# Kernel tuning notes

Measured on AMD Instinct MI355X. Metric: run time of the kernel, lower is better.

## Reference

```python
import jax, jax.numpy as jnp
import numpy as np

NEG_SLOPE = 0.2
NUM_GRAPHS = 64


def _gatv2_layer(x, src, dst, Wl, bl, Wr, br, att, bias, n_nodes, heads, ch):
    # lin_l (source) and lin_r (target) transforms -> [N, H, C]
    xs = (x @ Wl + bl).reshape(n_nodes, heads, ch)
    xd = (x @ Wr + br).reshape(n_nodes, heads, ch)
    s = xs[src]                                   # [E, H, C] gathered source feats
    e = jax.nn.leaky_relu(s + xd[dst], NEG_SLOPE)  # GATv2: leaky_relu BEFORE att dot
    score = jnp.einsum('ehc,hc->eh', e, att)       # [E, H]
    # segment softmax over edges sharing the same target node
    smax = jax.ops.segment_max(score, dst, num_segments=n_nodes)
    ex = jnp.exp(score - smax[dst])
    denom = jax.ops.segment_sum(ex, dst, num_segments=n_nodes)
    alpha = ex / denom[dst]                        # [E, H]
    out = jax.ops.segment_sum(alpha[:, :, None] * s, dst, num_segments=n_nodes)
    return out.reshape(n_nodes, heads * ch) + bias


def setup_inputs() -> dict:
    key = jax.random.key(0)
    ks = jax.random.split(key, 20)
    N, E, F = 50000, 800000, 128
    H, C = 4, 64
    G = NUM_GRAPHS
    sc = 0.05
    inp = {
        'x': jax.random.normal(ks[0], (N, F), jnp.float32),
        'edge_index': jax.random.randint(ks[1], (2, E), 0, N, jnp.int64 if jax.config.read('jax_enable_x64') else jnp.int32).astype(jnp.int32),
        'batch': jnp.sort(jax.random.randint(ks[2], (N,), 0, G)).astype(jnp.int32),
        'W_l1': jax.random.normal(ks[3], (F, H * C)) * sc,
        'b_l1': jax.random.normal(ks[4], (H * C,)) * sc,
        'W_r1': jax.random.normal(ks[5], (F, H * C)) * sc,
        'b_r1': jax.random.normal(ks[6], (H * C,)) * sc,
        'att1': jax.random.normal(ks[7], (H, C)) * sc,
        'bias1': jax.random.normal(ks[8], (H * C,)) * sc,
        'W_l2': jax.random.normal(ks[9], (H * C, C)) * sc,
        'b_l2': jax.random.normal(ks[10], (C,)) * sc,
        'W_r2': jax.random.normal(ks[11], (H * C, C)) * sc,
        'b_r2': jax.random.normal(ks[12], (C,)) * sc,
        'att2': jax.random.normal(ks[13], (1, C)) * sc,
        'bias2': jax.random.normal(ks[14], (C,)) * sc,
        'W_lin': jax.random.normal(ks[15], (C, 1)) * sc,
        'b_lin': jax.random.normal(ks[16], (1,)) * sc,
    }
    return inp


def reference(x, edge_index, batch, W_l1, b_l1, W_r1, b_r1, att1, bias1,
              W_l2, b_l2, W_r2, b_r2, att2, bias2, W_lin, b_lin):
    N = x.shape[0]
    # PyG GATv2Conv adds self-loops by default
    loops = jnp.arange(N, dtype=edge_index.dtype)
    src = jnp.concatenate([edge_index[0], loops])
    dst = jnp.concatenate([edge_index[1], loops])

    h = _gatv2_layer(x, src, dst, W_l1, b_l1, W_r1, b_r1, att1, bias1, N, 4, 64)
    h = jax.nn.relu(h)  # dropout=identity (eval), norm=Identity
    h = _gatv2_layer(h, src, dst, W_l2, b_l2, W_r2, b_r2, att2, bias2, N, 1, 64)

    # global mean pool over graphs
    sums = jax.ops.segment_sum(h, batch, num_segments=NUM_GRAPHS)
    counts = jax.ops.segment_sum(jnp.ones((N,), h.dtype), batch, num_segments=NUM_GRAPHS)
    pooled = sums / jnp.maximum(counts, 1.0)[:, None]  # [G, 64]
    return pooled @ W_lin + b_lin                      # [G, 1]
```

## Files before the change

kernel.cpp:

```cpp
#include <hip/hip_runtime.h>
#include <hip/hip_bf16.h>
#include <math.h>

typedef __attribute__((ext_vector_type(8))) short short8;
typedef __attribute__((ext_vector_type(4))) float floatx4;
typedef __attribute__((ext_vector_type(4))) int intx4;

#define ATT_SCALE 0.865617024533378f
#define C_ABS 0.6666666666667f
#define PCLAMP 86.5f

__device__ __forceinline__ float bf2f(unsigned short u) {
  union { unsigned int i; float f; } v; v.i = ((unsigned int)u) << 16; return v.f;
}
__device__ __forceinline__ unsigned short f2bf(float f) {
  union { float f; unsigned int u; } v; v.f = f;
  unsigned int r = (v.u + 0x7fffu + ((v.u >> 16) & 1u)) >> 16;
  return (unsigned short)r;
}
__device__ __forceinline__ int imin(int a, int b) { return a < b ? a : b; }
__device__ __forceinline__ int iclamp(int v, int lo, int hi) {
  return v < lo ? lo : (v > hi ? hi : v);
}
__device__ __forceinline__ float uasf(unsigned int u) {
  union { unsigned int i; float f; } v; v.i = u; return v.f;
}
__device__ __forceinline__ float exp2fast(float x) {
#if __has_builtin(__builtin_amdgcn_exp2f)
  return __builtin_amdgcn_exp2f(x);
#else
  return exp2f(x);
#endif
}
__device__ __forceinline__ float sum16(float x) {
  union { float f; int i; } a, t;
  a.f = x;
  t.i = __builtin_amdgcn_update_dpp(0, a.i, 0x121, 0xF, 0xF, true); a.f += t.f;
  t.i = __builtin_amdgcn_update_dpp(0, a.i, 0x122, 0xF, 0xF, true); a.f += t.f;
  t.i = __builtin_amdgcn_update_dpp(0, a.i, 0x124, 0xF, 0xF, true); a.f += t.f;
  t.i = __builtin_amdgcn_update_dpp(0, a.i, 0x128, 0xF, 0xF, true); a.f += t.f;
  return a.f;
}

__global__ void k_sentinel(float* out, float val) {
  if (threadIdx.x < 64) out[threadIdx.x] = val;
}

struct CvtSegs {
  const void* src[10];
  unsigned short* dst[10];
  int len[10];
};

__global__ void k_prep(const void* __restrict__ x, unsigned short* __restrict__ x_c,
                       int n8, CvtSegs segs,
                       const void* __restrict__ s0, const void* __restrict__ s1,
                       const void* __restrict__ s2, const void* __restrict__ s3,
                       unsigned short* __restrict__ d0, unsigned short* __restrict__ d1,
                       unsigned short* __restrict__ d2, unsigned short* __restrict__ d3,
                       const int* __restrict__ edst, int* deg, int E, int N,
                       int* dflag, float* __restrict__ att1s, float* __restrict__ att2s,
                       int nCvt8, int nTransB) {
  __shared__ int csh;
  if (threadIdx.x == 0) csh = 0;
  __syncthreads();
  {
    unsigned short u = ((const unsigned short*)x)[threadIdx.x];
    int e = (u >> 7) & 0xFF;
    atomicAdd(&csh, (u == 0) || (e >= 100 && e <= 145));
  }
  __syncthreads();
  int isf = (csh < 240);

  int b = blockIdx.x;
  if (b < nCvt8) {
    if (!isf) return;
    int i = b * 256 + threadIdx.x;
    if (i >= n8) return;
    const float* s = (const float*)x + (size_t)i * 8;
    ushort4 a, c;
    a.x = f2bf(s[0]); a.y = f2bf(s[1]); a.z = f2bf(s[2]); a.w = f2bf(s[3]);
    c.x = f2bf(s[4]); c.y = f2bf(s[5]); c.z = f2bf(s[6]); c.w = f2bf(s[7]);
    ((ushort4*)x_c)[i * 2] = a;
    ((ushort4*)x_c)[i * 2 + 1] = c;
    return;
  }
  b -= nCvt8;
  if (b < 10) {
    if (b == 0 && threadIdx.x == 0) dflag[0] = isf;
    int i = threadIdx.x;
    if (i < segs.len[b]) {
      float v = isf ? ((const float*)segs.src[b])[i]
                    : bf2f(((const unsigned short*)segs.src[b])[i]);
      segs.dst[b][i] = f2bf(v);
      if (b == 2) att1s[i] = v * ATT_SCALE;
      if (b == 6) att2s[i] = v * ATT_SCALE;
    }
    return;
  }
  b -= 10;
  if (b < nTransB) {
    int idx = b * 256 + threadIdx.x;
    const void* src; unsigned short* dst; int R, C, loc;
    if (idx < 32768)      { src = s0; dst = d0; R = 128; C = 256; loc = idx; }
    else if (idx < 65536) { src = s1; dst = d1; R = 128; C = 256; loc = idx - 32768; }
    else if (idx < 81920) { src = s2; dst = d2; R = 256; C = 64;  loc = idx - 65536; }
    else                  { src = s3; dst = d3; R = 256; C = 64;  loc = idx - 81920; }
    unsigned short u = isf ? f2bf(((const float*)src)[loc])
                           : ((const unsigned short*)src)[loc];
    int r = loc / C, cc = loc - r * C;
    dst[cc * R + r] = u;
    return;
  }
  b -= nTransB;
  int base = b * 1024 + threadIdx.x;
#pragma unroll
  for (int k = 0; k < 4; ++k) {
    int e = base + k * 256;
    if (e < E) atomicAdd(&deg[iclamp(edst[e], 0, N - 1)], 1);
  }
}

__global__ __launch_bounds__(1024) void k_scan1(const int* __restrict__ deg, int* bsum, int N) {
  __shared__ int sm[1024];
  int tid = threadIdx.x;
  int i = blockIdx.x * 1024 + tid;
  sm[tid] = (i < N) ? ((deg[i] + 4) & ~3) : 0;
  __syncthreads();
  for (int off = 512; off > 0; off >>= 1) {
    if (tid < off) sm[tid] += sm[tid + off];
    __syncthreads();
  }
  if (tid == 0) bsum[blockIdx.x] = sm[0];
}

__global__ __launch_bounds__(1024) void k_scan3(const int* __restrict__ deg,
                                                const int* __restrict__ bsum,
                                                int* rowptr, int* cursor, int N) {
  __shared__ int sm[1024];
  __shared__ int boff;
  int tid = threadIdx.x;
  if (tid == 0) {
    int r = 0;
    for (int b = 0; b < blockIdx.x; ++b) r += bsum[b];
    boff = r;
  }
  int i = blockIdx.x * 1024 + tid;
  int v = (i < N) ? ((deg[i] + 4) & ~3) : 0;
  sm[tid] = v;
  __syncthreads();
  for (int off = 1; off < 1024; off <<= 1) {
    int t = (tid >= off) ? sm[tid - off] : 0;
    __syncthreads();
    sm[tid] += t;
    __syncthreads();
  }
  if (i < N) {
    int ex = sm[tid] - v + boff;
    rowptr[i] = ex;
    cursor[i] = ex;
    if (i == N - 1) rowptr[N] = ex + v;
  }
}

template <int K, int CT, int RT>
__device__ __forceinline__ void gemm2r_body(
    int bx, int by, int tid,
    const unsigned short* __restrict__ A,
    const unsigned short* __restrict__ BTl, const unsigned short* __restrict__ BTr,
    const unsigned short* __restrict__ bl, const unsigned short* __restrict__ br,
    unsigned short* __restrict__ outl, unsigned short* __restrict__ outr,
    int Nrows, int M) {
  constexpr int KI = K / 32;
  int lane = tid & 63;
  int wave = tid >> 6;
  int r = lane & 15, q = lane >> 4;
  int col0 = by * (4 * CT * 16) + wave * (CT * 16);
  int row0 = bx * (16 * RT);
  short8 Bl[KI][CT], Br[KI][CT];
#pragma unroll
  for (int t = 0; t < CT; ++t) {
    const unsigned short* bpl = BTl + (size_t)(col0 + t * 16 + r) * K + q * 8;
    const unsigned short* bpr = BTr + (size_t)(col0 + t * 16 + r) * K + q * 8;
#pragma unroll
    for (int k = 0; k < KI; ++k) {
      Bl[k][t] = *reinterpret_cast<const short8*>(bpl + k * 32);
      Br[k][t] = *reinterpret_cast<const short8*>(bpr + k * 32);
    }
  }
  float bvl[CT], bvr[CT];
#pragma unroll
  for (int t = 0; t < CT; ++t) {
    bvl[t] = bf2f(bl[col0 + t * 16 + r]);
    bvr[t] = bf2f(br[col0 + t * 16 + r]);
  }
  short8 a[KI], an[KI];
  {
    int ar0 = imin(row0 + r, Nrows - 1);
    const unsigned short* Ap = A + (size_t)ar0 * K + q * 8;
#pragma unroll
    for (int k = 0; k < KI; ++k) a[k] = *reinterpret_cast<const short8*>(Ap + k * 32);
  }
  for (int rt = 0; rt < RT; ++rt) {
    if (rt + 1 < RT) {
      int arn = imin(row0 + (rt + 1) * 16 + r, Nrows - 1);
      const unsigned short* Apn = A + (size_t)arn * K + q * 8;
#pragma unroll
      for (int k = 0; k < KI; ++k) an[k] = *reinterpret_cast<const short8*>(Apn + k * 32);
    }
    floatx4 accl[CT], accr[CT];
#pragma unroll
    for (int t = 0; t < CT; ++t) {
      accl[t] = (floatx4){0.f, 0.f, 0.f, 0.f};
      accr[t] = (floatx4){0.f, 0.f, 0.f, 0.f};
    }
#pragma unroll
    for (int k = 0; k < KI; ++k) {
#pragma unroll
      for (int t = 0; t < CT; ++t) {
        accl[t] = __builtin_amdgcn_mfma_f32_16x16x32_bf16(a[k], Bl[k][t], accl[t], 0, 0, 0);
        accr[t] = __builtin_amdgcn_mfma_f32_16x16x32_bf16(a[k], Br[k][t], accr[t], 0, 0, 0);
      }
    }
#pragma unroll
    for (int t = 0; t < CT; ++t) {
      int col = col0 + t * 16 + r;
#pragma unroll
      for (int rr = 0; rr < 4; ++rr) {
        int row = row0 + rt * 16 + q * 4 + rr;
        if (row < Nrows) {
          outl[(size_t)row * M + col] = f2bf(accl[t][rr] + bvl[t]);
          outr[(size_t)row * M + col] = f2bf(accr[t][rr] + bvr[t]);
        }
      }
    }
#pragma unroll
    for (int k = 0; k < KI; ++k) a[k] = an[k];
  }
}

__global__ __launch_bounds__(256) void k_phase1(
    const unsigned short* __restrict__ A0, const unsigned short* __restrict__ A1,
    const int* __restrict__ dflag,
    const unsigned short* __restrict__ BTl, const unsigned short* __restrict__ BTr,
    const unsigned short* __restrict__ bl, const unsigned short* __restrict__ br,
    unsigned short* __restrict__ outl, unsigned short* __restrict__ outr,
    int Nrows, int M, int nG, int nS,
    const int* __restrict__ esrc, const int* __restrict__ edst,
    const int* __restrict__ rowptr, const int* __restrict__ deg,
    int* cursor, int* colx, int E, int N) {
  int b = blockIdx.x;
  int m2 = 2 * imin(nG, nS);
  bool isG;
  int idx;
  if (b < m2) { isG = (b & 1) == 0; idx = b >> 1; }
  else        { isG = nG > nS;      idx = imin(nG, nS) + (b - m2); }
  if (isG) {
    const unsigned short* A = dflag[0] ? A1 : A0;
    gemm2r_body<128, 2, 8>(idx >> 1, idx & 1, threadIdx.x, A, BTl, BTr, bl, br,
                           outl, outr, Nrows, M);
    return;
  }
  int ET = E + N;
  int ETcap = E + 4 * N;
  int base = idx * 1024 + threadIdx.x;
#pragma unroll
  for (int k = 0; k < 4; ++k) {
    int e = base + k * 256;
    if (e < ET) {
      if (e < E) {
        int s = iclamp(esrc[e], 0, N - 1), d = iclamp(edst[e], 0, N - 1);
        int pos = atomicAdd(&cursor[d], 1);
        colx[iclamp(pos, 0, ETcap - 1)] = s;
      } else {
        int i = e - E;
        int bg = rowptr[i];
        int en = bg + deg[i];
        colx[en] = i;
        int cap = rowptr[i + 1];
        for (int j = en + 1; j < cap; ++j) colx[j] = 0;
        if (i == N - 1) {
          for (int j = cap; j < cap + 16; ++j) colx[j] = 0;
        }
      }
    }
  }
}

__global__ __launch_bounds__(256) void k_gemm2r_l2(
    const unsigned short* __restrict__ A,
    const unsigned short* __restrict__ BTl, const unsigned short* __restrict__ BTr,
    const unsigned short* __restrict__ bl, const unsigned short* __restrict__ br,
    unsigned short* __restrict__ outl, unsigned short* __restrict__ outr,
    int Nrows, int M) {
  gemm2r_body<256, 1, 4>(blockIdx.x, 0, threadIdx.x, A, BTl, BTr, bl, br,
                         outl, outr, Nrows, M);
}

#define UNPACK2(u, v0, v1, v2, v3)          \
  v0 = uasf(u.x << 16); v1 = uasf(u.x & 0xffff0000u); \
  v2 = uasf(u.y << 16); v3 = uasf(u.y & 0xffff0000u);

#define AGG4(U0, U1, U2, U3, E0, F0)                                         \
  {                                                                          \
    float va0, va1, va2, va3, vb0, vb1, vb2, vb3;                            \
    float vc0, vc1, vc2, vc3, vd0, vd1, vd2, vd3;                            \
    UNPACK2(U0, va0, va1, va2, va3)                                          \
    UNPACK2(U1, vb0, vb1, vb2, vb3)                                          \
    UNPACK2(U2, vc0, vc1, vc2, vc3)                                          \
    UNPACK2(U3, vd0, vd1, vd2, vd3)                                          \
    float qa0 = fmaf(a0, va0, ad0), qa1 = fmaf(a1, va1, ad1);                \
    float qa2 = fmaf(a2, va2, ad2), qa3 = fmaf(a3, va3, ad3);                \
    float qb0 = fmaf(a0, vb0, ad0), qb1 = fmaf(a1, vb1, ad1);                \
    float qb2 = fmaf(a2, vb2, ad2), qb3 = fmaf(a3, vb3, ad3);                \
    float qc0 = fmaf(a0, vc0, ad0), qc1 = fmaf(a1, vc1, ad1);                \
    float qc2 = fmaf(a2, vc2, ad2), qc3 = fmaf(a3, vc3, ad3);                \
    float qd0 = fmaf(a0, vd0, ad0), qd1 = fmaf(a1, vd1, ad1);                \
    float qd2 = fmaf(a2, vd2, ad2), qd3 = fmaf(a3, vd3, ad3);                \
    float pa = (qa0 + qa1) + (qa2 + qa3);                                    \
    float pb = (qb0 + qb1) + (qb2 + qb3);                                    \
    float pc = (qc0 + qc1) + (qc2 + qc3);                                    \
    float pd = (qd0 + qd1) + (qd2 + qd3);                                    \
    pa = fmaf(c0, fabsf(qa0), pa); pa = fmaf(c1, fabsf(qa1), pa);            \
    pa = fmaf(c2, fabsf(qa2), pa); pa = fmaf(c3, fabsf(qa3), pa);            \
    pb = fmaf(c0, fabsf(qb0), pb); pb = fmaf(c1, fabsf(qb1), pb);            \
    pb = fmaf(c2, fabsf(qb2), pb); pb = fmaf(c3, fabsf(qb3), pb);            \
    pc = fmaf(c0, fabsf(qc0), pc); pc = fmaf(c1, fabsf(qc1), pc);            \
    pc = fmaf(c2, fabsf(qc2), pc); pc = fmaf(c3, fabsf(qc3), pc);            \
    pd = fmaf(c0, fabsf(qd0), pd); pd = fmaf(c1, fabsf(qd1), pd);            \
    pd = fmaf(c2, fabsf(qd2), pd); pd = fmaf(c3, fabsf(qd3), pd);            \
    pa = sum16(pa); pb = sum16(pb); pc = sum16(pc); pd = sum16(pd);          \
    float l0 = (F0) ? PCLAMP : (((E0) < end) ? PCLAMP : -INFINITY);          \
    float l1 = ((E0) + 1 < end) ? PCLAMP : -INFINITY;                        \
    float l2 = ((E0) + 2 < end) ? PCLAMP : -INFINITY;                        \
    float l3 = ((E0) + 3 < end) ? PCLAMP : -INFINITY;                        \
    pa = fminf(pa, l0); pb = fminf(pb, l1);                                  \
    pc = fminf(pc, l2); pd = fminf(pd, l3);                                  \
    float wa = exp2fast(pa), wb = exp2fast(pb);                              \
    float wc = exp2fast(pc), wd = exp2fast(pd);                              \
    l += (wa + wb) + (wc + wd);                                              \
    o0 = fmaf(wa, va0, o0); o0 = fmaf(wb, vb0, o0);                          \
    o0 = fmaf(wc, vc0, o0); o0 = fmaf(wd, vd0, o0);                          \
    o1 = fmaf(wa, va1, o1); o1 = fmaf(wb, vb1, o1);                          \
    o1 = fmaf(wc, vc1, o1); o1 = fmaf(wd, vd1, o1);                          \
    o2 = fmaf(wa, va2, o2); o2 = fmaf(wb, vb2, o2);                          \
    o2 = fmaf(wc, vc2, o2); o2 = fmaf(wd, vd2, o2);                          \
    o3 = fmaf(wa, va3, o3); o3 = fmaf(wb, vb3, o3);                          \
    o3 = fmaf(wc, vc3, o3); o3 = fmaf(wd, vd3, o3);                          \
  }

__global__ __launch_bounds__(256, 6) void k_agg_h4(
    const int* __restrict__ rowptr, const int* __restrict__ deg,
    const int* __restrict__ colx,
    const unsigned short* __restrict__ xs, const unsigned short* __restrict__ xd,
    const float* __restrict__ atts, const unsigned short* __restrict__ bias,
    unsigned short* __restrict__ hout, int N) {
  int lane = threadIdx.x & 63;
  int dst = (blockIdx.x * 256 + threadIdx.x) >> 6;
  if (dst >= N) return;
  int off = lane << 2;
  unsigned int off2 = (unsigned int)off * 2;
  const char* xsb = (const char*)xs;
  floatx4 av = *reinterpret_cast<const floatx4*>(atts + off);
  ushort4 du = *reinterpret_cast<const ushort4*>(xd + (size_t)dst * 256 + off);
  float a0 = av[0], a1 = av[1], a2 = av[2], a3 = av[3];
  float d0 = bf2f(du.x), d1 = bf2f(du.y), d2 = bf2f(du.z), d3 = bf2f(du.w);
  float ad0 = a0 * d0, ad1 = a1 * d1, ad2 = a2 * d2, ad3 = a3 * d3;
  float c0 = copysignf(C_ABS, a0), c1 = copysignf(C_ABS, a1);
  float c2 = copysignf(C_ABS, a2), c3 = copysignf(C_ABS, a3);
  float l = 0.f, o0 = 0.f, o1 = 0.f, o2 = 0.f, o3 = 0.f;
  int beg = __builtin_amdgcn_readfirstlane(rowptr[dst]);
  int cnt = __builtin_amdgcn_readfirstlane(deg[dst]) + 1;
  int end = beg + cnt;
#define GATH(p) (*(const uint2*)(xsb + (((unsigned)(p) << 9) + off2)))
  intx4 pA = *(const intx4*)(colx + beg);
  intx4 pB = *(const intx4*)(colx + beg + 4);
  uint2 ua = GATH(pA.x), ub = GATH(pA.y), uc = GATH(pA.z), ud = GATH(pA.w);
  uint2 ue = GATH(pB.x), uf = GATH(pB.y), ug = GATH(pB.z), uh = GATH(pB.w);
  for (int e = beg; e < end; e += 8) {
    intx4 pC = *(const intx4*)(colx + e + 8);
    intx4 pD = *(const intx4*)(colx + e + 12);
    AGG4(ua, ub, uc, ud, e, 1)
    ua = GATH(pC.x); ub = GATH(pC.y); uc = GATH(pC.z); ud = GATH(pC.w);
    AGG4(ue, uf, ug, uh, e + 4, 0)
    ue = GATH(pD.x); uf = GATH(pD.y); ug = GATH(pD.z); uh = GATH(pD.w);
  }
#undef GATH
  float rl = 1.0f / l;
  ushort4 bu = *reinterpret_cast<const ushort4*>(bias + off);
  ushort4 res;
  res.x = f2bf(fmaxf(fmaf(o0, rl, bf2f(bu.x)), 0.f));
  res.y = f2bf(fmaxf(fmaf(o1, rl, bf2f(bu.y)), 0.f));
  res.z = f2bf(fmaxf(fmaf(o2, rl, bf2f(bu.z)), 0.f));
  res.w = f2bf(fmaxf(fmaf(o3, rl, bf2f(bu.w)), 0.f));
  *reinterpret_cast<ushort4*>(hout + (size_t)dst * 256 + off) = res;
}

__global__ __launch_bounds__(256, 6) void k_agg_h1(
    const int* __restrict__ rowptr, const int* __restrict__ deg,
    const int* __restrict__ colx,
    const unsigned short* __restrict__ xs, const unsigned short* __restrict__ xd,
    const float* __restrict__ atts, const unsigned short* __restrict__ bias,
    float* __restrict__ hout, int N) {
  int lane = threadIdx.x & 63;
  int wid = (blockIdx.x * 256 + threadIdx.x) >> 6;
  int g = lane >> 4, sl = lane & 15;
  int dst = wid * 4 + g;
  bool valid = dst < N;
  int dsafe = valid ? dst : 0;
  int cb = sl << 2;
  unsigned int cb2 = (unsigned int)cb * 2;
  const char* xsb = (const char*)xs;
  floatx4 av = *reinterpret_cast<const floatx4*>(atts + cb);
  ushort4 du = *reinterpret_cast<const ushort4*>(xd + (size_t)dsafe * 64 + cb);
  float a0 = av[0], a1 = av[1], a2 = av[2], a3 = av[3];
  float d0 = bf2f(du.x), d1 = bf2f(du.y), d2 = bf2f(du.z), d3 = bf2f(du.w);
  float ad0 = a0 * d0, ad1 = a1 * d1, ad2 = a2 * d2, ad3 = a3 * d3;
  float c0 = copysignf(C_ABS, a0), c1 = copysignf(C_ABS, a1);
  float c2 = copysignf(C_ABS, a2), c3 = copysignf(C_ABS, a3);
  float l = 0.f, o0 = 0.f, o1 = 0.f, o2 = 0.f, o3 = 0.f;
  int beg = valid ? rowptr[dst] : 0;
  int end = beg + (valid ? deg[dst] + 1 : 0);
#define GATH(p) (*(const uint2*)(xsb + (((unsigned)(p) << 7) + cb2)))
  intx4 pA = *(const intx4*)(colx + beg);
  intx4 pB = *(const intx4*)(colx + beg + 4);
  uint2 ua = GATH(pA.x), ub = GATH(pA.y), uc = GATH(pA.z), ud = GATH(pA.w);
  uint2 ue = GATH(pB.x), uf = GATH(pB.y), ug = GATH(pB.z), uh = GATH(pB.w);
  for (int e = beg; e < end; e += 8) {
    intx4 pC = *(const intx4*)(colx + e + 8);
    intx4 pD = *(const intx4*)(colx + e + 12);
    AGG4(ua, ub, uc, ud, e, 1)
    ua = GATH(pC.x); ub = GATH(pC.y); uc = GATH(pC.z); ud = GATH(pC.w);
    AGG4(ue, uf, ug, uh, e + 4, 0)
    ue = GATH(pD.x); uf = GATH(pD.y); ug = GATH(pD.z); uh = GATH(pD.w);
  }
#undef GATH
  if (valid) {
    float rl = 1.0f / l;
    ushort4 bu = *reinterpret_cast<const ushort4*>(bias + cb);
    floatx4 res;
    res[0] = fmaf(o0, rl, bf2f(bu.x));
    res[1] = fmaf(o1, rl, bf2f(bu.y));
    res[2] = fmaf(o2, rl, bf2f(bu.z));
    res[3] = fmaf(o3, rl, bf2f(bu.w));
    *reinterpret_cast<floatx4*>(hout + (size_t)dst * 64 + cb) = res;
  }
}

__global__ __launch_bounds__(256) void k_pool(const float* __restrict__ h2,
                                              const int* __restrict__ batch,
                                              float* pool, int* cnt, int N) {
  int lane = threadIdx.x & 63;
  int wid = (blockIdx.x * 256 + threadIdx.x) >> 6;
  int n0 = wid * 32;
  if (n0 >= N) return;
  int nend = imin(n0 + 32, N);
  float acc = 0.f;
  int c = 0;
  int gcur = iclamp(batch[n0], 0, 63);
  for (int n = n0; n < nend; ++n) {
    int gg = iclamp(batch[n], 0, 63);
    if (gg != gcur) {
      atomicAdd(&pool[gcur * 64 + lane], acc);
      if (lane == 0) atomicAdd(&cnt[gcur], c);
      acc = 0.f; c = 0; gcur = gg;
    }
    acc += h2[(size_t)n * 64 + lane];
    c++;
  }
  atomicAdd(&pool[gcur * 64 + lane], acc);
  if (lane == 0) atomicAdd(&cnt[gcur], c);
}

__global__ void k_final(const float* __restrict__ pool, const int* __restrict__ cnt,
                        const unsigned short* __restrict__ Wlinc,
                        const unsigned short* __restrict__ blinc,
                        float* __restrict__ out) {
  int g = threadIdx.x;
  if (g >= 64) return;
  float inv = 1.f / fmaxf((float)cnt[g], 1.f);
  float s = 0.f;
  for (int c = 0; c < 64; ++c) s += pool[g * 64 + c] * bf2f(Wlinc[c]);
  out[g] = fmaf(s, inv, bf2f(blinc[0]));
}

extern "C" void kernel_launch(void* const* d_in, const int* in_sizes, int n_in,
                              void* d_out, int out_size, void* d_ws, size_t ws_size,
                              hipStream_t stream) {
  const void* x     = d_in[0];
  const int*  ei    = (const int*)d_in[1];
  const int*  batch = (const int*)d_in[2];
  const void* Wl1 = d_in[3];  const void* bl1 = d_in[4];
  const void* Wr1 = d_in[5];  const void* br1 = d_in[6];
  const void* att1 = d_in[7]; const void* bias1 = d_in[8];
  const void* Wl2 = d_in[9];  const void* bl2 = d_in[10];
  const void* Wr2 = d_in[11]; const void* br2 = d_in[12];
  const void* att2 = d_in[13]; const void* bias2 = d_in[14];
  const void* Wlin = d_in[15]; const void* blin = d_in[16];
  float* out = (float*)d_out;

  const int F = 128, HC = 256, C2 = 64;
  int N = in_sizes[0] / F;
  int E = in_sizes[1] / 2;
  int ET = E + N;
  const int* esrc = ei;
  const int* edst = ei + E;

  char* w = (char*)d_ws;
  auto alloc = [&](size_t bytes) {
    char* p = w;
    w += (bytes + 255) & ~(size_t)255;
    return p;
  };
  int* dflag  = (int*)alloc(4);
  int* rowptr = (int*)alloc((size_t)(N + 1) * 4);
  int* cursor = (int*)alloc((size_t)N * 4);
  int* bsum   = (int*)alloc(1024 * 4);
  int* colx   = (int*)alloc((size_t)(E + 4 * N + 16) * 4);
  unsigned short* smallc = (unsigned short*)alloc(4096);
  float* att1s = (float*)alloc(256 * 4);
  float* att2s = (float*)alloc(64 * 4);
  unsigned short* Wl1T = (unsigned short*)alloc((size_t)F * HC * 2);
  unsigned short* Wr1T = (unsigned short*)alloc((size_t)F * HC * 2);
  unsigned short* Wl2T = (unsigned short*)alloc((size_t)HC * C2 * 2);
  unsigned short* Wr2T = (unsigned short*)alloc((size_t)HC * C2 * 2);
  int* deg    = (int*)alloc((size_t)N * 4);
  float* pool = (float*)alloc(64 * 64 * 4);
  int* cnt    = (int*)alloc(64 * 4);
  unsigned short* xs1  = (unsigned short*)alloc((size_t)N * HC * 2);
  unsigned short* xd1  = (unsigned short*)alloc((size_t)N * HC * 2);
  unsigned short* h1   = (unsigned short*)alloc((size_t)N * HC * 2);
  size_t required = (size_t)(w - (char*)d_ws);
  size_t zlen = (size_t)((char*)cnt + 256 - (char*)deg);

  unsigned short* x_c = h1;
  unsigned short* xs2 = xs1;
  unsigned short* xd2 = xs1 + (size_t)N * C2;
  float*          h2  = (float*)xd1;

  unsigned short* bl1c   = smallc + 0;
  unsigned short* br1c   = smallc + 256;
  unsigned short* att1c  = smallc + 512;
  unsigned short* bias1c = smallc + 768;
  unsigned short* bl2c   = smallc + 1024;
  unsigned short* br2c   = smallc + 1088;
  unsigned short* att2c  = smallc + 1152;
  unsigned short* bias2c = smallc + 1216;
  unsigned short* Wlinc  = smallc + 1280;
  unsigned short* blinc  = smallc + 1344;

  if (ws_size < required) {
    k_sentinel<<<1, 64, 0, stream>>>(out, 1000.f + (float)(ws_size >> 20));
    return;
  }

  hipMemsetAsync(deg, 0, zlen, stream);

  CvtSegs segs;
  const void* ssrc[10] = {bl1, br1, att1, bias1, bl2, br2, att2, bias2, Wlin, blin};
  unsigned short* sdst[10] = {bl1c, br1c, att1c, bias1c, bl2c, br2c, att2c, bias2c, Wlinc, blinc};
  int slen[10] = {256, 256, 256, 256, 64, 64, 64, 64, 64, 1};
  for (int i = 0; i < 10; ++i) { segs.src[i] = ssrc[i]; segs.dst[i] = sdst[i]; segs.len[i] = slen[i]; }
  int n8 = N * F / 8;
  int nCvt8 = (n8 + 255) / 256;
  int nTransB = (2 * F * HC + 2 * HC * C2 + 255) / 256;
  int nHist = (E + 1023) / 1024;
  k_prep<<<nCvt8 + 10 + nTransB + nHist, 256, 0, stream>>>(
      x, x_c, n8, segs, Wl1, Wr1, Wl2, Wr2, Wl1T, Wr1T, Wl2T, Wr2T,
      edst, deg, E, N, dflag, att1s, att2s, nCvt8, nTransB);

  int nb = (N + 1023) / 1024;
  k_scan1<<<nb, 1024, 0, stream>>>(deg, bsum, N);
  k_scan3<<<nb, 1024, 0, stream>>>(deg, bsum, rowptr, cursor, N);

  int nG = ((N + 127) / 128) * 2;
  int nS = (ET + 1023) / 1024;
  k_phase1<<<nG + nS, 256, 0, stream>>>(
      (const unsigned short*)x, x_c, dflag, Wl1T, Wr1T, bl1c, br1c, xs1, xd1,
      N, HC, nG, nS, esrc, edst, rowptr, deg, cursor, colx, E, N);

  k_agg_h4<<<(N + 3) / 4, 256, 0, stream>>>(rowptr, deg, colx, xs1, xd1, att1s, bias1c, h1, N);

  k_gemm2r_l2<<<(N + 63) / 64, 256, 0, stream>>>(h1, Wl2T, Wr2T, bl2c, br2c, xs2, xd2, N, C2);
  k_agg_h1<<<(N + 15) / 16, 256, 0, stream>>>(rowptr, deg, colx, xs2, xd2, att2s, bias2c, h2, N);

  int pw = (N + 31) / 32;
  k_pool<<<(pw + 3) / 4, 256, 0, stream>>>(h2, batch, pool, cnt, N);
  k_final<<<1, 64, 0, stream>>>(pool, cnt, Wlinc, blinc, out);
}
```

Measured before the change: 333.6 us.

## Degree-sort destination nodes and widen per-lane vectors in GATv2 aggregation

Builds a histogram of node in-degrees during the scan kernels and uses a counting sort in phase1 to produce a degree-sorted order of destination nodes. The aggregation kernels then process nodes in that order, so nodes sharing a wave have similar edge counts and less divergence. Each lane now handles 8 channels with 16-byte gathers (2 destinations per wave for layer 1, 8 for layer 2), and the row reduction drops from 16 lanes to 8. This adds extra atomics, a second memset for colx padding, and an indirection through order. It also loses the wave-uniform readfirstlane loop bounds the layer-1 kernel had before.

New measurement: 345.4 us. 1.04x slower.

```diff
diff --git a/kernel.cpp b/kernel.cpp
--- a/kernel.cpp
+++ b/kernel.cpp
@@ -32,13 +32,12 @@
   return exp2f(x);
 #endif
 }
-__device__ __forceinline__ float sum16(float x) {
+__device__ __forceinline__ float sum8(float x) {
   union { float f; int i; } a, t;
   a.f = x;
-  t.i = __builtin_amdgcn_update_dpp(0, a.i, 0x121, 0xF, 0xF, true); a.f += t.f;
-  t.i = __builtin_amdgcn_update_dpp(0, a.i, 0x122, 0xF, 0xF, true); a.f += t.f;
-  t.i = __builtin_amdgcn_update_dpp(0, a.i, 0x124, 0xF, 0xF, true); a.f += t.f;
-  t.i = __builtin_amdgcn_update_dpp(0, a.i, 0x128, 0xF, 0xF, true); a.f += t.f;
+  t.i = __builtin_amdgcn_update_dpp(0, a.i, 0xB1, 0xF, 0xF, true); a.f += t.f;
+  t.i = __builtin_amdgcn_update_dpp(0, a.i, 0x4E, 0xF, 0xF, true); a.f += t.f;
+  t.i = __builtin_amdgcn_ds_swizzle(a.i, 0x101F); a.f += t.f;
   return a.f;
 }
 
@@ -121,24 +120,34 @@
   }
 }
 
-__global__ __launch_bounds__(1024) void k_scan1(const int* __restrict__ deg, int* bsum, int N) {
+__global__ __launch_bounds__(1024) void k_scan1(const int* __restrict__ deg, int* bsum,
+                                                int* dhist, int N) {
   __shared__ int sm[1024];
+  __shared__ int lh[256];
   int tid = threadIdx.x;
+  if (tid < 256) lh[tid] = 0;
+  __syncthreads();
   int i = blockIdx.x * 1024 + tid;
-  sm[tid] = (i < N) ? ((deg[i] + 4) & ~3) : 0;
+  int d = (i < N) ? deg[i] : 0;
+  if (i < N) atomicAdd(&lh[imin(d, 255)], 1);
+  sm[tid] = (i < N) ? ((d + 4) & ~3) : 0;
   __syncthreads();
   for (int off = 512; off > 0; off >>= 1) {
     if (tid < off) sm[tid] += sm[tid + off];
     __syncthreads();
   }
   if (tid == 0) bsum[blockIdx.x] = sm[0];
+  if (tid < 256 && lh[tid]) atomicAdd(&dhist[tid], lh[tid]);
 }
 
 __global__ __launch_bounds__(1024) void k_scan3(const int* __restrict__ deg,
                                                 const int* __restrict__ bsum,
+                                                const int* __restrict__ dhist,
+                                                int* dcur,
                                                 int* rowptr, int* cursor, int N) {
   __shared__ int sm[1024];
   __shared__ int boff;
+  __shared__ int hsc[256];
   int tid = threadIdx.x;
   if (tid == 0) {
     int r = 0;
@@ -161,6 +170,17 @@
     cursor[i] = ex;
     if (i == N - 1) rowptr[N] = ex + v;
   }
+  int hv = 0;
+  if (blockIdx.x == 0 && tid < 256) { hv = dhist[tid]; hsc[tid] = hv; }
+  __syncthreads();
+  for (int off = 1; off < 256; off <<= 1) {
+    int t = 0;
+    if (blockIdx.x == 0 && tid < 256 && tid >= off) t = hsc[tid - off];
+    __syncthreads();
+    if (blockIdx.x == 0 && tid < 256) hsc[tid] += t;
+    __syncthreads();
+  }
+  if (blockIdx.x == 0 && tid < 256) dcur[tid] = hsc[tid] - hv;
 }
 
 template <int K, int CT, int RT>
@@ -248,7 +268,7 @@
     int Nrows, int M, int nG, int nS,
     const int* __restrict__ esrc, const int* __restrict__ edst,
     const int* __restrict__ rowptr, const int* __restrict__ deg,
-    int* cursor, int* colx, int E, int N) {
+    int* cursor, int* colx, int* dcur, int* order, int E, int N) {
   int b = blockIdx.x;
   int m2 = 2 * imin(nG, nS);
   bool isG;
@@ -261,30 +281,41 @@
                            outl, outr, Nrows, M);
     return;
   }
+  __shared__ int scnt[256];
+  __shared__ int sbase[256];
   int ET = E + N;
   int ETcap = E + 4 * N;
   int base = idx * 1024 + threadIdx.x;
+  if (threadIdx.x < 256) scnt[threadIdx.x] = 0;
+  __syncthreads();
 #pragma unroll
   for (int k = 0; k < 4; ++k) {
     int e = base + k * 256;
-    if (e < ET) {
-      if (e < E) {
-        int s = iclamp(esrc[e], 0, N - 1), d = iclamp(edst[e], 0, N - 1);
-        int pos = atomicAdd(&cursor[d], 1);
-        colx[iclamp(pos, 0, ETcap - 1)] = s;
-      } else {
-        int i = e - E;
-        int bg = rowptr[i];
-        int en = bg + deg[i];
-        colx[en] = i;
-        int cap = rowptr[i + 1];
-        for (int j = en + 1; j < cap; ++j) colx[j] = 0;
-        if (i == N - 1) {
-          for (int j = cap; j < cap + 16; ++j) colx[j] = 0;
-        }
-      }
-    }
-  }
+    if (e < E) {
+      int s = iclamp(esrc[e], 0, N - 1), d = iclamp(edst[e], 0, N - 1);
+      int pos = atomicAdd(&cursor[d], 1);
+      colx[iclamp(pos, 0, ETcap - 1)] = s;
+    }
+  }
+  bool n0 = false, n1 = false, n2 = false, n3 = false;
+  int i0 = 0, i1 = 0, i2 = 0, i3 = 0, b0 = 0, b1 = 0, b2 = 0, b3 = 0;
+  int l0 = 0, l1 = 0, l2 = 0, l3 = 0;
+#define NODEK(nk, ik, bk, lk, KK) { int e = base + KK * 256;                  \
+    if (e >= E && e < ET) { int i = e - E; int bg = rowptr[i]; int dv = deg[i]; \
+      colx[bg + dv] = i; int cap = rowptr[i + 1];                             \
+      for (int j = bg + dv + 1; j < cap; ++j) colx[j] = 0;                    \
+      ik = i; bk = imin(dv, 255); lk = atomicAdd(&scnt[bk], 1); nk = true; } }
+  NODEK(n0, i0, b0, l0, 0) NODEK(n1, i1, b1, l1, 1)
+  NODEK(n2, i2, b2, l2, 2) NODEK(n3, i3, b3, l3, 3)
+#undef NODEK
+  __syncthreads();
+  if (threadIdx.x < 256 && scnt[threadIdx.x])
+    sbase[threadIdx.x] = atomicAdd(&dcur[threadIdx.x], scnt[threadIdx.x]);
+  __syncthreads();
+  if (n0) order[sbase[b0] + l0] = i0;
+  if (n1) order[sbase[b1] + l1] = i1;
+  if (n2) order[sbase[b2] + l2] = i2;
+  if (n3) order[sbase[b3] + l3] = i3;
 }
 
 __global__ __launch_bounds__(256) void k_gemm2r_l2(
@@ -297,154 +328,132 @@
                          outl, outr, Nrows, M);
 }
 
-#define UNPACK2(u, v0, v1, v2, v3)          \
-  v0 = uasf(u.x << 16); v1 = uasf(u.x & 0xffff0000u); \
-  v2 = uasf(u.y << 16); v3 = uasf(u.y & 0xffff0000u);
-
-#define AGG4(U0, U1, U2, U3, E0, F0)                                         \
+#define AGG1(U, KK, REM)                                                     \
   {                                                                          \
-    float va0, va1, va2, va3, vb0, vb1, vb2, vb3;                            \
-    float vc0, vc1, vc2, vc3, vd0, vd1, vd2, vd3;                            \
-    UNPACK2(U0, va0, va1, va2, va3)                                          \
-    UNPACK2(U1, vb0, vb1, vb2, vb3)                                          \
-    UNPACK2(U2, vc0, vc1, vc2, vc3)                                          \
-    UNPACK2(U3, vd0, vd1, vd2, vd3)                                          \
-    float qa0 = fmaf(a0, va0, ad0), qa1 = fmaf(a1, va1, ad1);                \
-    float qa2 = fmaf(a2, va2, ad2), qa3 = fmaf(a3, va3, ad3);                \
-    float qb0 = fmaf(a0, vb0, ad0), qb1 = fmaf(a1, vb1, ad1);                \
-    float qb2 = fmaf(a2, vb2, ad2), qb3 = fmaf(a3, vb3, ad3);                \
-    float qc0 = fmaf(a0, vc0, ad0), qc1 = fmaf(a1, vc1, ad1);                \
-    float qc2 = fmaf(a2, vc2, ad2), qc3 = fmaf(a3, vc3, ad3);                \
-    float qd0 = fmaf(a0, vd0, ad0), qd1 = fmaf(a1, vd1, ad1);                \
-    float qd2 = fmaf(a2, vd2, ad2), qd3 = fmaf(a3, vd3, ad3);                \
-    float pa = (qa0 + qa1) + (qa2 + qa3);                                    \
-    float pb = (qb0 + qb1) + (qb2 + qb3);                                    \
-    float pc = (qc0 + qc1) + (qc2 + qc3);                                    \
-    float pd = (qd0 + qd1) + (qd2 + qd3);                                    \
-    pa = fmaf(c0, fabsf(qa0), pa); pa = fmaf(c1, fabsf(qa1), pa);            \
-    pa = fmaf(c2, fabsf(qa2), pa); pa = fmaf(c3, fabsf(qa3), pa);            \
-    pb = fmaf(c0, fabsf(qb0), pb); pb = fmaf(c1, fabsf(qb1), pb);            \
-    pb = fmaf(c2, fabsf(qb2), pb); pb = fmaf(c3, fabsf(qb3), pb);            \
-    pc = fmaf(c0, fabsf(qc0), pc); pc = fmaf(c1, fabsf(qc1), pc);            \
-    pc = fmaf(c2, fabsf(qc2), pc); pc = fmaf(c3, fabsf(qc3), pc);            \
-    pd = fmaf(c0, fabsf(qd0), pd); pd = fmaf(c1, fabsf(qd1), pd);            \
-    pd = fmaf(c2, fabsf(qd2), pd); pd = fmaf(c3, fabsf(qd3), pd);            \
-    pa = sum16(pa); pb = sum16(pb); pc = sum16(pc); pd = sum16(pd);          \
-    float l0 = (F0) ? PCLAMP : (((E0) < end) ? PCLAMP : -INFINITY);          \
-    float l1 = ((E0) + 1 < end) ? PCLAMP : -INFINITY;                        \
-    float l2 = ((E0) + 2 < end) ? PCLAMP : -INFINITY;                        \
-    float l3 = ((E0) + 3 < end) ? PCLAMP : -INFINITY;                        \
-    pa = fminf(pa, l0); pb = fminf(pb, l1);                                  \
-    pc = fminf(pc, l2); pd = fminf(pd, l3);                                  \
-    float wa = exp2fast(pa), wb = exp2fast(pb);                              \
-    float wc = exp2fast(pc), wd = exp2fast(pd);                              \
-    l += (wa + wb) + (wc + wd);                                              \
-    o0 = fmaf(wa, va0, o0); o0 = fmaf(wb, vb0, o0);                          \
-    o0 = fmaf(wc, vc0, o0); o0 = fmaf(wd, vd0, o0);                          \
-    o1 = fmaf(wa, va1, o1); o1 = fmaf(wb, vb1, o1);                          \
-    o1 = fmaf(wc, vc1, o1); o1 = fmaf(wd, vd1, o1);                          \
-    o2 = fmaf(wa, va2, o2); o2 = fmaf(wb, vb2, o2);                          \
-    o2 = fmaf(wc, vc2, o2); o2 = fmaf(wd, vd2, o2);                          \
-    o3 = fmaf(wa, va3, o3); o3 = fmaf(wb, vb3, o3);                          \
-    o3 = fmaf(wc, vc3, o3); o3 = fmaf(wd, vd3, o3);                          \
-  }
-
-__global__ __launch_bounds__(256, 6) void k_agg_h4(
+    float v0 = uasf(U.x << 16), v1 = uasf(U.x & 0xffff0000u);                \
+    float v2 = uasf(U.y << 16), v3 = uasf(U.y & 0xffff0000u);                \
+    float v4 = uasf(U.z << 16), v5 = uasf(U.z & 0xffff0000u);                \
+    float v6 = uasf(U.w << 16), v7 = uasf(U.w & 0xffff0000u);                \
+    float q0 = fmaf(a0, v0, ad0), q1 = fmaf(a1, v1, ad1);                    \
+    float q2 = fmaf(a2, v2, ad2), q3 = fmaf(a3, v3, ad3);                    \
+    float q4 = fmaf(a4, v4, ad4), q5 = fmaf(a5, v5, ad5);                    \
+    float q6 = fmaf(a6, v6, ad6), q7 = fmaf(a7, v7, ad7);                    \
+    float p = ((q0 + q1) + (q2 + q3)) + ((q4 + q5) + (q6 + q7));             \
+    p = fmaf(c0, fabsf(q0), p); p = fmaf(c1, fabsf(q1), p);                  \
+    p = fmaf(c2, fabsf(q2), p); p = fmaf(c3, fabsf(q3), p);                  \
+    p = fmaf(c4, fabsf(q4), p); p = fmaf(c5, fabsf(q5), p);                  \
+    p = fmaf(c6, fabsf(q6), p); p = fmaf(c7, fabsf(q7), p);                  \
+    p = sum8(p);                                                             \
+    float lim = (KK < (REM)) ? PCLAMP : -INFINITY;                           \
+    p = fminf(p, lim);                                                       \
+    float w = exp2fast(p);                                                   \
+    l += w;                                                                  \
+    o0 = fmaf(w, v0, o0); o1 = fmaf(w, v1, o1);                              \
+    o2 = fmaf(w, v2, o2); o3 = fmaf(w, v3, o3);                              \
+    o4 = fmaf(w, v4, o4); o5 = fmaf(w, v5, o5);                              \
+    o6 = fmaf(w, v6, o6); o7 = fmaf(w, v7, o7);                              \
+  }
+
+template <int LOG_ROWB, int LPD_LOG, bool BF16_RELU_OUT>
+__device__ __forceinline__ void agg_body(
     const int* __restrict__ rowptr, const int* __restrict__ deg,
-    const int* __restrict__ colx,
+    const int* __restrict__ colx, const int* __restrict__ order,
+    const unsigned short* __restrict__ xs, const unsigned short* __restrict__ xd,
+    const float* __restrict__ atts, const unsigned short* __restrict__ bias,
+    void* __restrict__ hout, int N) {
+  int lane = threadIdx.x & 63;
+  int wid = (blockIdx.x * 256 + threadIdx.x) >> 6;
+  constexpr int LPD = 1 << LPD_LOG;
+  constexpr int DPW = 64 >> LPD_LOG;
+  int g = lane >> LPD_LOG;
+  int s = lane & (LPD - 1);
+  int di = wid * DPW + g;
+  bool valid = di < N;
+  int dst = valid ? order[di] : 0;
+  int beg = valid ? rowptr[dst] : 0;
+  int lenv = valid ? deg[dst] + 1 : 0;
+  unsigned int lb = (unsigned int)s * 16;
+  int ch0 = s * 8;
+  const char* xsb = (const char*)xs;
+  floatx4 avl = *(const floatx4*)(atts + ch0);
+  floatx4 avh = *(const floatx4*)(atts + ch0 + 4);
+  uint4 du = *(const uint4*)((const char*)xd + ((size_t)dst << LOG_ROWB) + lb);
+  float a0 = avl[0], a1 = avl[1], a2 = avl[2], a3 = avl[3];
+  float a4 = avh[0], a5 = avh[1], a6 = avh[2], a7 = avh[3];
+  float d0 = uasf(du.x << 16), d1 = uasf(du.x & 0xffff0000u);
+  float d2 = uasf(du.y << 16), d3 = uasf(du.y & 0xffff0000u);
+  float d4 = uasf(du.z << 16), d5 = uasf(du.z & 0xffff0000u);
+  float d6 = uasf(du.w << 16), d7 = uasf(du.w & 0xffff0000u);
+  float ad0 = a0 * d0, ad1 = a1 * d1, ad2 = a2 * d2, ad3 = a3 * d3;
+  float ad4 = a4 * d4, ad5 = a5 * d5, ad6 = a6 * d6, ad7 = a7 * d7;
+  float c0 = copysignf(C_ABS, a0), c1 = copysignf(C_ABS, a1);
+  float c2 = copysignf(C_ABS, a2), c3 = copysignf(C_ABS, a3);
+  float c4 = copysignf(C_ABS, a4), c5 = copysignf(C_ABS, a5);
+  float c6 = copysignf(C_ABS, a6), c7 = copysignf(C_ABS, a7);
+  float l = 0.f;
+  float o0 = 0.f, o1 = 0.f, o2 = 0.f, o3 = 0.f;
+  float o4 = 0.f, o5 = 0.f, o6 = 0.f, o7 = 0.f;
+  const int* cx = colx + beg;
+#define GATH(p) (*(const uint4*)(xsb + (((unsigned)(p) << LOG_ROWB) + lb)))
+  intx4 qA = *(const intx4*)(cx);
+  intx4 qB = *(const intx4*)(cx + 4);
+  uint4 uA0 = GATH(qA.x), uA1 = GATH(qA.y), uA2 = GATH(qA.z), uA3 = GATH(qA.w);
+  uint4 uB0 = GATH(qB.x), uB1 = GATH(qB.y), uB2 = GATH(qB.z), uB3 = GATH(qB.w);
+  for (int e = 0; e < lenv; e += 8) {
+    intx4 qC = *(const intx4*)(cx + e + 8);
+    intx4 qD = *(const intx4*)(cx + e + 12);
+    int rem = lenv - e;
+    AGG1(uA0, 0, rem) AGG1(uA1, 1, rem) AGG1(uA2, 2, rem) AGG1(uA3, 3, rem)
+    uA0 = GATH(qC.x); uA1 = GATH(qC.y); uA2 = GATH(qC.z); uA3 = GATH(qC.w);
+    int rem4 = rem - 4;
+    AGG1(uB0, 0, rem4) AGG1(uB1, 1, rem4) AGG1(uB2, 2, rem4) AGG1(uB3, 3, rem4)
+    uB0 = GATH(qD.x); uB1 = GATH(qD.y); uB2 = GATH(qD.z); uB3 = GATH(qD.w);
+  }
+#undef GATH
+  if (!valid) return;
+  float rl = 1.0f / l;
+  uint4 bu = *(const uint4*)((const char*)bias + lb);
+  float b0 = uasf(bu.x << 16), b1 = uasf(bu.x & 0xffff0000u);
+  float b2 = uasf(bu.y << 16), b3 = uasf(bu.y & 0xffff0000u);
+  float b4 = uasf(bu.z << 16), b5 = uasf(bu.z & 0xffff0000u);
+  float b6 = uasf(bu.w << 16), b7 = uasf(bu.w & 0xffff0000u);
+  float r0 = fmaf(o0, rl, b0), r1 = fmaf(o1, rl, b1);
+  float r2 = fmaf(o2, rl, b2), r3 = fmaf(o3, rl, b3);
+  float r4 = fmaf(o4, rl, b4), r5 = fmaf(o5, rl, b5);
+  float r6 = fmaf(o6, rl, b6), r7 = fmaf(o7, rl, b7);
+  if constexpr (BF16_RELU_OUT) {
+    r0 = fmaxf(r0, 0.f); r1 = fmaxf(r1, 0.f); r2 = fmaxf(r2, 0.f); r3 = fmaxf(r3, 0.f);
+    r4 = fmaxf(r4, 0.f); r5 = fmaxf(r5, 0.f); r6 = fmaxf(r6, 0.f); r7 = fmaxf(r7, 0.f);
+    uint4 res;
+    res.x = (unsigned)f2bf(r0) | ((unsigned)f2bf(r1) << 16);
+    res.y = (unsigned)f2bf(r2) | ((unsigned)f2bf(r3) << 16);
+    res.z = (unsigned)f2bf(r4) | ((unsigned)f2bf(r5) << 16);
+    res.w = (unsigned)f2bf(r6) | ((unsigned)f2bf(r7) << 16);
+    *(uint4*)((char*)hout + ((size_t)dst << LOG_ROWB) + lb) = res;
+  } else {
+    floatx4 ra = {r0, r1, r2, r3}, rb = {r4, r5, r6, r7};
+    char* op = (char*)hout + (size_t)dst * 256 + (unsigned)ch0 * 4;
+    *(floatx4*)op = ra;
+    *(floatx4*)(op + 16) = rb;
+  }
+}
+
+__global__ __launch_bounds__(256) void k_agg_h4(
+    const int* __restrict__ rowptr, const int* __restrict__ deg,
+    const int* __restrict__ colx, const int* __restrict__ order,
     const unsigned short* __restrict__ xs, const unsigned short* __restrict__ xd,
     const float* __restrict__ atts, const unsigned short* __restrict__ bias,
     unsigned short* __restrict__ hout, int N) {
-  int lane = threadIdx.x & 63;
-  int dst = (blockIdx.x * 256 + threadIdx.x) >> 6;
-  if (dst >= N) return;
-  int off = lane << 2;
-  unsigned int off2 = (unsigned int)off * 2;
-  const char* xsb = (const char*)xs;
-  floatx4 av = *reinterpret_cast<const floatx4*>(atts + off);
-  ushort4 du = *reinterpret_cast<const ushort4*>(xd + (size_t)dst * 256 + off);
-  float a0 = av[0], a1 = av[1], a2 = av[2], a3 = av[3];
-  float d0 = bf2f(du.x), d1 = bf2f(du.y), d2 = bf2f(du.z), d3 = bf2f(du.w);
-  float ad0 = a0 * d0, ad1 = a1 * d1, ad2 = a2 * d2, ad3 = a3 * d3;
-  float c0 = copysignf(C_ABS, a0), c1 = copysignf(C_ABS, a1);
-  float c2 = copysignf(C_ABS, a2), c3 = copysignf(C_ABS, a3);
-  float l = 0.f, o0 = 0.f, o1 = 0.f, o2 = 0.f, o3 = 0.f;
-  int beg = __builtin_amdgcn_readfirstlane(rowptr[dst]);
-  int cnt = __builtin_amdgcn_readfirstlane(deg[dst]) + 1;
-  int end = beg + cnt;
-#define GATH(p) (*(const uint2*)(xsb + (((unsigned)(p) << 9) + off2)))
-  intx4 pA = *(const intx4*)(colx + beg);
-  intx4 pB = *(const intx4*)(colx + beg + 4);
-  uint2 ua = GATH(pA.x), ub = GATH(pA.y), uc = GATH(pA.z), ud = GATH(pA.w);
-  uint2 ue = GATH(pB.x), uf = GATH(pB.y), ug = GATH(pB.z), uh = GATH(pB.w);
-  for (int e = beg; e < end; e += 8) {
-    intx4 pC = *(const intx4*)(colx + e + 8);
-    intx4 pD = *(const intx4*)(colx + e + 12);
-    AGG4(ua, ub, uc, ud, e, 1)
-    ua = GATH(pC.x); ub = GATH(pC.y); uc = GATH(pC.z); ud = GATH(pC.w);
-    AGG4(ue, uf, ug, uh, e + 4, 0)
-    ue = GATH(pD.x); uf = GATH(pD.y); ug = GATH(pD.z); uh = GATH(pD.w);
-  }
-#undef GATH
-  float rl = 1.0f / l;
-  ushort4 bu = *reinterpret_cast<const ushort4*>(bias + off);
-  ushort4 res;
-  res.x = f2bf(fmaxf(fmaf(o0, rl, bf2f(bu.x)), 0.f));
-  res.y = f2bf(fmaxf(fmaf(o1, rl, bf2f(bu.y)), 0.f));
-  res.z = f2bf(fmaxf(fmaf(o2, rl, bf2f(bu.z)), 0.f));
-  res.w = f2bf(fmaxf(fmaf(o3, rl, bf2f(bu.w)), 0.f));
-  *reinterpret_cast<ushort4*>(hout + (size_t)dst * 256 + off) = res;
-}
-
-__global__ __launch_bounds__(256, 6) void k_agg_h1(
+  agg_body<9, 5, true>(rowptr, deg, colx, order, xs, xd, atts, bias, hout, N);
+}
+
+__global__ __launch_bounds__(256) void k_agg_h1(
     const int* __restrict__ rowptr, const int* __restrict__ deg,
-    const int* __restrict__ colx,
+    const int* __restrict__ colx, const int* __restrict__ order,
     const unsigned short* __restrict__ xs, const unsigned short* __restrict__ xd,
     const float* __restrict__ atts, const unsigned short* __restrict__ bias,
     float* __restrict__ hout, int N) {
-  int lane = threadIdx.x & 63;
-  int wid = (blockIdx.x * 256 + threadIdx.x) >> 6;
-  int g = lane >> 4, sl = lane & 15;
-  int dst = wid * 4 + g;
-  bool valid = dst < N;
-  int dsafe = valid ? dst : 0;
-  int cb = sl << 2;
-  unsigned int cb2 = (unsigned int)cb * 2;
-  const char* xsb = (const char*)xs;
-  floatx4 av = *reinterpret_cast<const floatx4*>(atts + cb);
-  ushort4 du = *reinterpret_cast<const ushort4*>(xd + (size_t)dsafe * 64 + cb);
-  float a0 = av[0], a1 = av[1], a2 = av[2], a3 = av[3];
-  float d0 = bf2f(du.x), d1 = bf2f(du.y), d2 = bf2f(du.z), d3 = bf2f(du.w);
-  float ad0 = a0 * d0, ad1 = a1 * d1, ad2 = a2 * d2, ad3 = a3 * d3;
-  float c0 = copysignf(C_ABS, a0), c1 = copysignf(C_ABS, a1);
-  float c2 = copysignf(C_ABS, a2), c3 = copysignf(C_ABS, a3);
-  float l = 0.f, o0 = 0.f, o1 = 0.f, o2 = 0.f, o3 = 0.f;
-  int beg = valid ? rowptr[dst] : 0;
-  int end = beg + (valid ? deg[dst] + 1 : 0);
-#define GATH(p) (*(const uint2*)(xsb + (((unsigned)(p) << 7) + cb2)))
-  intx4 pA = *(const intx4*)(colx + beg);
-  intx4 pB = *(const intx4*)(colx + beg + 4);
-  uint2 ua = GATH(pA.x), ub = GATH(pA.y), uc = GATH(pA.z), ud = GATH(pA.w);
-  uint2 ue = GATH(pB.x), uf = GATH(pB.y), ug = GATH(pB.z), uh = GATH(pB.w);
-  for (int e = beg; e < end; e += 8) {
-    intx4 pC = *(const intx4*)(colx + e + 8);
-    intx4 pD = *(const intx4*)(colx + e + 12);
-    AGG4(ua, ub, uc, ud, e, 1)
-    ua = GATH(pC.x); ub = GATH(pC.y); uc = GATH(pC.z); ud = GATH(pC.w);
-    AGG4(ue, uf, ug, uh, e + 4, 0)
-    ue = GATH(pD.x); uf = GATH(pD.y); ug = GATH(pD.z); uh = GATH(pD.w);
-  }
-#undef GATH
-  if (valid) {
-    float rl = 1.0f / l;
-    ushort4 bu = *reinterpret_cast<const ushort4*>(bias + cb);
-    floatx4 res;
-    res[0] = fmaf(o0, rl, bf2f(bu.x));
-    res[1] = fmaf(o1, rl, bf2f(bu.y));
-    res[2] = fmaf(o2, rl, bf2f(bu.z));
-    res[3] = fmaf(o3, rl, bf2f(bu.w));
-    *reinterpret_cast<floatx4*>(hout + (size_t)dst * 64 + cb) = res;
-  }
+  agg_body<7, 3, false>(rowptr, deg, colx, order, xs, xd, atts, bias, hout, N);
 }
 
 __global__ __launch_bounds__(256) void k_pool(const float* __restrict__ h2,
@@ -516,7 +525,8 @@
   int* rowptr = (int*)alloc((size_t)(N + 1) * 4);
   int* cursor = (int*)alloc((size_t)N * 4);
   int* bsum   = (int*)alloc(1024 * 4);
-  int* colx   = (int*)alloc((size_t)(E + 4 * N + 16) * 4);
+  int* colx   = (int*)alloc((size_t)(E + 4 * N + 1024 + 16) * 4);
+  int* order  = (int*)alloc((size_t)N * 4);
   unsigned short* smallc = (unsigned short*)alloc(4096);
   float* att1s = (float*)alloc(256 * 4);
   float* att2s = (float*)alloc(64 * 4);
@@ -527,11 +537,13 @@
   int* deg    = (int*)alloc((size_t)N * 4);
   float* pool = (float*)alloc(64 * 64 * 4);
   int* cnt    = (int*)alloc(64 * 4);
+  int* dhist  = (int*)alloc(256 * 4);
+  int* dcur   = (int*)alloc(256 * 4);
   unsigned short* xs1  = (unsigned short*)alloc((size_t)N * HC * 2);
   unsigned short* xd1  = (unsigned short*)alloc((size_t)N * HC * 2);
   unsigned short* h1   = (unsigned short*)alloc((size_t)N * HC * 2);
   size_t required = (size_t)(w - (char*)d_ws);
-  size_t zlen = (size_t)((char*)cnt + 256 - (char*)deg);
+  size_t zlen = (size_t)((char*)dcur + 1024 - (char*)deg);
 
   unsigned short* x_c = h1;
   unsigned short* xs2 = xs1;
@@ -555,6 +567,7 @@
   }
 
   hipMemsetAsync(deg, 0, zlen, stream);
+  hipMemsetAsync(colx + (size_t)E + N, 0, ((size_t)3 * N + 1024 + 16) * 4, stream);
 
   CvtSegs segs;
   const void* ssrc[10] = {bl1, br1, att1, bias1, bl2, br2, att2, bias2, Wlin, blin};
@@ -570,19 +583,21 @@
       edst, deg, E, N, dflag, att1s, att2s, nCvt8, nTransB);
 
   int nb = (N + 1023) / 1024;
-  k_scan1<<<nb, 1024, 0, stream>>>(deg, bsum, N);
-  k_scan3<<<nb, 1024, 0, stream>>>(deg, bsum, rowptr, cursor, N);
+  k_scan1<<<nb, 1024, 0, stream>>>(deg, bsum, dhist, N);
+  k_scan3<<<nb, 1024, 0, stream>>>(deg, bsum, dhist, dcur, rowptr, cursor, N);
 
   int nG = ((N + 127) / 128) * 2;
   int nS = (ET + 1023) / 1024;
   k_phase1<<<nG + nS, 256, 0, stream>>>(
       (const unsigned short*)x, x_c, dflag, Wl1T, Wr1T, bl1c, br1c, xs1, xd1,
-      N, HC, nG, nS, esrc, edst, rowptr, deg, cursor, colx, E, N);
-
-  k_agg_h4<<<(N + 3) / 4, 256, 0, stream>>>(rowptr, deg, colx, xs1, xd1, att1s, bias1c, h1, N);
+      N, HC, nG, nS, esrc, edst, rowptr, deg, cursor, colx, dcur, order, E, N);
+
+  k_agg_h4<<<(N + 7) / 8, 256, 0, stream>>>(rowptr, deg, colx, order, xs1, xd1,
+                                            att1s, bias1c, h1, N);
 
   k_gemm2r_l2<<<(N + 63) / 64, 256, 0, stream>>>(h1, Wl2T, Wr2T, bl2c, br2c, xs2, xd2, N, C2);
-  k_agg_h1<<<(N + 15) / 16, 256, 0, stream>>>(rowptr, deg, colx, xs2, xd2, att2s, bias2c, h2, N);
+  k_agg_h1<<<(N + 31) / 32, 256, 0, stream>>>(rowptr, deg, colx, order, xs2, xd2,
+                                              att2s, bias2c, h2, N);
 
   int pw = (N + 31) / 32;
   k_pool<<<(pw + 3) / 4, 256, 0, stream>>>(h2, batch, pool, cnt, N);
```
